# Performance work log

Hardware: AMD Instinct MI355X
Metric: run time of the kernel (lower is better)

Reference implementation:

```python
import jax, jax.numpy as jnp
import numpy as np

N = 50000
E = 800000
C = 128   # embed_channels
H = 4     # num_heads
D = C // H
POS = 3


def setup_inputs() -> dict:
    key = jax.random.key(0)
    ks = jax.random.split(key, 8)
    feat = jax.random.normal(ks[0], (N, C), dtype=jnp.float32)
    coord = jax.random.normal(ks[1], (N, POS), dtype=jnp.float32)
    graph = jax.random.randint(ks[2], (2, E), 0, N, dtype=jnp.int32)
    qkv_w = jax.random.normal(ks[3], (3 * C, C), dtype=jnp.float32) * (1.0 / np.sqrt(C))
    qkv_b = jax.random.normal(ks[4], (3 * C,), dtype=jnp.float32) * 0.02
    rpe_w = jax.random.normal(ks[5], (C, POS), dtype=jnp.float32) * (1.0 / np.sqrt(POS))
    rpe_b = jax.random.normal(ks[6], (C,), dtype=jnp.float32) * 0.02
    return {"feat": feat, "coord": coord, "graph": graph,
            "qkv_w": qkv_w, "qkv_b": qkv_b, "rpe_w": rpe_w, "rpe_b": rpe_b}


def _segment_softmax(x, seg, n):
    # x: [E, H], seg: [E] -> softmax over edges sharing the same destination node
    seg_max = jax.ops.segment_max(x, seg, num_segments=n)          # [N, H]
    seg_max = jnp.where(jnp.isfinite(seg_max), seg_max, 0.0)
    ex = jnp.exp(x - seg_max[seg])                                 # [E, H]
    seg_sum = jax.ops.segment_sum(ex, seg, num_segments=n)         # [N, H]
    return ex / seg_sum[seg]


def reference(feat, coord, graph, qkv_w, qkv_b, rpe_w, rpe_b):
    n = feat.shape[0]
    # qkv projection: [N, 3C] -> [N, 3, H, D]
    qkv = (feat @ qkv_w.T + qkv_b).reshape(n, 3, H, D)
    query, key, value = qkv[:, 0], qkv[:, 1], qkv[:, 2]            # each [N, H, D]
    dst, src = graph[0], graph[1]                                  # [E]
    # relative position encoding per edge
    rel = coord[dst] - coord[src]                                  # [E, 3]
    rpe = (rel @ rpe_w.T + rpe_b).reshape(-1, H, D)                # [E, H, D]
    # per-edge attention logits
    attn = (key[src] * query[dst] + rpe).sum(-1)                   # [E, H]
    attn = _segment_softmax(attn, dst, n)                          # [E, H]
    # weighted scatter-sum of values
    msg = attn[..., None] * value[src]                             # [E, H, D]
    out = jax.ops.segment_sum(msg, dst, num_segments=n)            # [N, H, D]
    return out.reshape(n, H * D)
```

## Files before the change

### kernel.cpp

```cpp
#include <hip/hip_runtime.h>
#include <hip/hip_bf16.h>

#define NN 50000
#define NE 800000
#define PAD 64
#define CONVB 6298

typedef _Float16 fp16x8 __attribute__((ext_vector_type(8)));
typedef _Float16 half2 __attribute__((ext_vector_type(2)));
typedef __attribute__((ext_vector_type(8))) unsigned short ushort8;
typedef __attribute__((ext_vector_type(4))) float f32x4;

static __device__ __forceinline__ unsigned short f2h(float x) {
    _Float16 h = (_Float16)x;
    return __builtin_bit_cast(unsigned short, h);
}
static __device__ __forceinline__ float dot2(half2 a, half2 b, float c) {
#if __has_builtin(__builtin_amdgcn_fdot2)
    return __builtin_amdgcn_fdot2(a, b, c, false);
#else
    return c + (float)a.x * (float)b.x + (float)a.y * (float)b.y;
#endif
}

__global__ __launch_bounds__(256) void k_pre(
    const float* __restrict__ feat, const float* __restrict__ w,
    unsigned short* __restrict__ feat16, unsigned short* __restrict__ w16,
    const float* __restrict__ coord, const float* __restrict__ rpe_w,
    const float* __restrict__ rpe_b, float* __restrict__ ca,
    float* __restrict__ cb)
{
    const int b = blockIdx.x;
    if (b < CONVB) {
        const int totalA = NN * 128 / 4;
        int idx = b * 256 + threadIdx.x;
        if (idx < totalA) {
            float4 a = ((const float4*)feat)[idx];
            ((ushort4*)feat16)[idx] = make_ushort4(f2h(a.x), f2h(a.y), f2h(a.z), f2h(a.w));
        } else {
            int k = idx - totalA;
            float4 a = ((const float4*)w)[k];
            ((ushort4*)w16)[k] = make_ushort4(f2h(a.x), f2h(a.y), f2h(a.z), f2h(a.w));
        }
        return;
    }
    __shared__ float s_rw[12];
    __shared__ float s_rb[4];
    if (threadIdx.x < 12) {
        int h = threadIdx.x / 3, p = threadIdx.x % 3;
        float s = 0.f;
        for (int d = 0; d < 32; ++d) s += rpe_w[(h * 32 + d) * 3 + p];
        s_rw[threadIdx.x] = s;
    } else if (threadIdx.x < 16) {
        int h = threadIdx.x - 12;
        float s = 0.f;
        for (int d = 0; d < 32; ++d) s += rpe_b[h * 32 + d];
        s_rb[h] = s;
    }
    __syncthreads();
    int n = (b - CONVB) * 256 + threadIdx.x;
    if (n < NN) {
        float c0 = coord[n * 3 + 0], c1 = coord[n * 3 + 1], c2 = coord[n * 3 + 2];
#pragma unroll
        for (int h = 0; h < 4; ++h) {
            float a = c0 * s_rw[h * 3 + 0] + c1 * s_rw[h * 3 + 1] + c2 * s_rw[h * 3 + 2];
            ca[n * 4 + h] = a;
            cb[n * 4 + h] = a + s_rb[h];
        }
    }
}

__global__ __launch_bounds__(256) void qkv_gemm(
    const unsigned short* __restrict__ feat16, const unsigned short* __restrict__ w16,
    const float* __restrict__ bias, unsigned short* __restrict__ qbuf16,
    unsigned short* __restrict__ kvbuf,
    const int* __restrict__ graph, int* __restrict__ cnt,
    int* __restrict__ sorted_src)
{
    const int role = blockIdx.x & 3;
    const int bi   = blockIdx.x >> 2;
    if (role == 3) {
        int t = threadIdx.x;
        for (int e = bi * 256 + t; e < NE; e += 391 * 256) {
            int dst = graph[e];
            int src = graph[NE + e];
            int slot = atomicAdd(&cnt[dst], 1);
            if (slot < PAD) sorted_src[(dst << 6) + slot] = src << 9;
        }
        return;
    }

    __shared__ __align__(16) unsigned short Ah[128][40];
    __shared__ __align__(16) unsigned short Bh[128][40];

    const int t  = threadIdx.x;
    const int bm = bi * 128;
    const int bc = role * 128;

    const int wave = t >> 6;
    const int lane = t & 63;
    const int wr = wave & 1;
    const int wc = wave >> 1;
    const int qd = lane >> 4;
    const int l15 = lane & 15;

    f32x4 acc[4][4];
#pragma unroll
    for (int i = 0; i < 4; ++i)
#pragma unroll
        for (int j = 0; j < 4; ++j)
            acc[i][j] = (f32x4){0.f, 0.f, 0.f, 0.f};

    for (int ks = 0; ks < 4; ++ks) {
        const int k0 = ks * 32;
        if (ks) __syncthreads();
#pragma unroll
        for (int c = 0; c < 2; ++c) {
            int idx = c * 256 + t;
            int r  = idx >> 2;
            int c8 = (idx & 3) * 8;
            int ga = bm + r;
            ushort8 a8 = (ga < NN)
                ? *(const ushort8*)(feat16 + (size_t)ga * 128 + k0 + c8)
                : (ushort8){0,0,0,0,0,0,0,0};
            *(ushort8*)&Ah[r][c8] = a8;
            *(ushort8*)&Bh[r][c8] = *(const ushort8*)(w16 + (size_t)(bc + r) * 128 + k0 + c8);
        }
        __syncthreads();
        fp16x8 af[4];
#pragma unroll
        for (int i = 0; i < 4; ++i)
            af[i] = *(const fp16x8*)&Ah[wr * 64 + 16 * i + l15][qd * 8];
#pragma unroll
        for (int j = 0; j < 4; ++j) {
            fp16x8 bf = *(const fp16x8*)&Bh[wc * 64 + 16 * j + l15][qd * 8];
#pragma unroll
            for (int i = 0; i < 4; ++i)
                acc[i][j] = __builtin_amdgcn_mfma_f32_16x16x32_f16(af[i], bf, acc[i][j], 0, 0, 0);
        }
    }

    float bj[4];
#pragma unroll
    for (int j = 0; j < 4; ++j)
        bj[j] = bias[bc + wc * 64 + 16 * j + l15];

    const int isQ = (role == 0);
    const int half = (role == 1) ? 0 : 128;
#pragma unroll
    for (int i = 0; i < 4; ++i) {
#pragma unroll
        for (int rg = 0; rg < 4; ++rg) {
            int row = bm + wr * 64 + 16 * i + qd * 4 + rg;
            if (row >= NN) continue;
#pragma unroll
            for (int j = 0; j < 4; ++j) {
                float v = acc[i][j][rg] + bj[j];
                int col = wc * 64 + 16 * j + l15;
                if (isQ) qbuf16[(size_t)row * 128 + col] = f2h(v);
                else     kvbuf[(size_t)row * 256 + half + col] = f2h(v);
            }
        }
    }
}

__global__ __launch_bounds__(256) void node_attn(
    const unsigned short* __restrict__ qbuf16, const unsigned short* __restrict__ kvbuf,
    const float* __restrict__ ca, const float* __restrict__ cb,
    const int* __restrict__ cnt, const int* __restrict__ sorted_src,
    float* __restrict__ out)
{
    const int t = threadIdx.x;
    const int n = blockIdx.x * 8 + (t >> 5);
    if (n >= NN) return;
    const int j = t & 31;
    const int h = j >> 3;
    const int j8 = j * 8;
    const int h4 = h * 4;

    const uint2 qv = *(const uint2*)((const char*)qbuf16 + (size_t)n * 256 + j8);
    const half2 qh01 = __builtin_bit_cast(half2, qv.x);
    const half2 qh23 = __builtin_bit_cast(half2, qv.y);
    const float cbh = cb[n * 4 + h];
    const int start = n << 6;
    int d = cnt[n];
    if (d > PAD) d = PAD;

    float4 acc = make_float4(0.f, 0.f, 0.f, 0.f);
    float den = 0.f;
    const char* kvp = (const char*)kvbuf;
    const char* cap = (const char*)ca;

    int i = 0;
    for (; i + 3 < d; i += 4) {
        int o0 = sorted_src[start + i];
        int o1 = sorted_src[start + i + 1];
        int o2 = sorted_src[start + i + 2];
        int o3 = sorted_src[start + i + 3];
        uint2 k0 = *(const uint2*)(kvp + (unsigned)o0 + j8);
        uint2 k1 = *(const uint2*)(kvp + (unsigned)o1 + j8);
        uint2 k2 = *(const uint2*)(kvp + (unsigned)o2 + j8);
        uint2 k3 = *(const uint2*)(kvp + (unsigned)o3 + j8);
        uint2 v0 = *(const uint2*)(kvp + (unsigned)o0 + 256 + j8);
        uint2 v1 = *(const uint2*)(kvp + (unsigned)o1 + 256 + j8);
        uint2 v2 = *(const uint2*)(kvp + (unsigned)o2 + 256 + j8);
        uint2 v3 = *(const uint2*)(kvp + (unsigned)o3 + 256 + j8);
        float a0 = *(const float*)(cap + ((unsigned)o0 >> 5) + h4);
        float a1 = *(const float*)(cap + ((unsigned)o1 >> 5) + h4);
        float a2 = *(const float*)(cap + ((unsigned)o2 >> 5) + h4);
        float a3 = *(const float*)(cap + ((unsigned)o3 >> 5) + h4);

        float p0 = dot2(qh01, __builtin_bit_cast(half2, k0.x),
                   dot2(qh23, __builtin_bit_cast(half2, k0.y), 0.f));
        float p1 = dot2(qh01, __builtin_bit_cast(half2, k1.x),
                   dot2(qh23, __builtin_bit_cast(half2, k1.y), 0.f));
        float p2 = dot2(qh01, __builtin_bit_cast(half2, k2.x),
                   dot2(qh23, __builtin_bit_cast(half2, k2.y), 0.f));
        float p3 = dot2(qh01, __builtin_bit_cast(half2, k3.x),
                   dot2(qh23, __builtin_bit_cast(half2, k3.y), 0.f));
        p0 += __shfl_xor(p0, 1); p1 += __shfl_xor(p1, 1);
        p2 += __shfl_xor(p2, 1); p3 += __shfl_xor(p3, 1);
        p0 += __shfl_xor(p0, 2); p1 += __shfl_xor(p1, 2);
        p2 += __shfl_xor(p2, 2); p3 += __shfl_xor(p3, 2);
        p0 += __shfl_xor(p0, 4); p1 += __shfl_xor(p1, 4);
        p2 += __shfl_xor(p2, 4); p3 += __shfl_xor(p3, 4);

        float e0 = __expf(p0 + cbh - a0);
        float e1 = __expf(p1 + cbh - a1);
        float e2 = __expf(p2 + cbh - a2);
        float e3 = __expf(p3 + cbh - a3);
        den += (e0 + e1) + (e2 + e3);
        half2 v0a = __builtin_bit_cast(half2, v0.x), v0b = __builtin_bit_cast(half2, v0.y);
        half2 v1a = __builtin_bit_cast(half2, v1.x), v1b = __builtin_bit_cast(half2, v1.y);
        half2 v2a = __builtin_bit_cast(half2, v2.x), v2b = __builtin_bit_cast(half2, v2.y);
        half2 v3a = __builtin_bit_cast(half2, v3.x), v3b = __builtin_bit_cast(half2, v3.y);
        acc.x += e0 * (float)v0a.x + e1 * (float)v1a.x + e2 * (float)v2a.x + e3 * (float)v3a.x;
        acc.y += e0 * (float)v0a.y + e1 * (float)v1a.y + e2 * (float)v2a.y + e3 * (float)v3a.y;
        acc.z += e0 * (float)v0b.x + e1 * (float)v1b.x + e2 * (float)v2b.x + e3 * (float)v3b.x;
        acc.w += e0 * (float)v0b.y + e1 * (float)v1b.y + e2 * (float)v2b.y + e3 * (float)v3b.y;
    }
    for (; i < d; ++i) {
        int o0 = sorted_src[start + i];
        uint2 k0 = *(const uint2*)(kvp + (unsigned)o0 + j8);
        uint2 v0 = *(const uint2*)(kvp + (unsigned)o0 + 256 + j8);
        float a0 = *(const float*)(cap + ((unsigned)o0 >> 5) + h4);
        float p0 = dot2(qh01, __builtin_bit_cast(half2, k0.x),
                   dot2(qh23, __builtin_bit_cast(half2, k0.y), 0.f));
        p0 += __shfl_xor(p0, 1);
        p0 += __shfl_xor(p0, 2);
        p0 += __shfl_xor(p0, 4);
        float e = __expf(p0 + cbh - a0);
        den += e;
        half2 va = __builtin_bit_cast(half2, v0.x);
        half2 vb = __builtin_bit_cast(half2, v0.y);
        acc.x += e * (float)va.x;
        acc.y += e * (float)va.y;
        acc.z += e * (float)vb.x;
        acc.w += e * (float)vb.y;
    }

    float inv = (den > 0.f) ? 1.0f / den : 0.f;
    float4 o = make_float4(acc.x * inv, acc.y * inv, acc.z * inv, acc.w * inv);
    ((float4*)(out + (size_t)n * 128))[j] = o;
}

extern "C" void kernel_launch(void* const* d_in, const int* in_sizes, int n_in,
                              void* d_out, int out_size, void* d_ws, size_t ws_size,
                              hipStream_t stream) {
    const float* feat  = (const float*)d_in[0];
    const float* coord = (const float*)d_in[1];
    const int*   graph = (const int*)d_in[2];
    const float* qkv_w = (const float*)d_in[3];
    const float* qkv_b = (const float*)d_in[4];
    const float* rpe_w = (const float*)d_in[5];
    const float* rpe_b = (const float*)d_in[6];
    float* out = (float*)d_out;

    unsigned short* qbuf16 = (unsigned short*)d_ws;
    unsigned short* kvbuf  = qbuf16 + (size_t)NN * 128;
    unsigned short* feat16 = kvbuf + (size_t)NN * 256;
    unsigned short* w16    = feat16 + (size_t)NN * 128;
    int*   cnt        = (int*)(w16 + 384 * 128);
    int*   sorted_src = cnt + NN;
    float* ca         = (float*)(sorted_src + (size_t)NN * PAD);
    float* cb         = ca + (size_t)NN * 4;

    hipMemsetAsync(cnt, 0, NN * sizeof(int), stream);

    k_pre    <<<dim3(CONVB + 196), 256, 0, stream>>>(feat, qkv_w, feat16, w16,
                                                     coord, rpe_w, rpe_b, ca, cb);
    qkv_gemm <<<dim3(391 * 4), 256, 0, stream>>>(feat16, w16, qkv_b, qbuf16, kvbuf,
                                                 graph, cnt, sorted_src);
    node_attn<<<dim3((NN + 7) / 8), 256, 0, stream>>>(qbuf16, kvbuf, ca, cb,
                                                      cnt, sorted_src, out);
}
```

Baseline: 214.2 us.

## Move edge bucketing into pre-kernel and stage GEMM output through LDS for vector stores

The edge-scatter work that builds per-destination source lists moves out of the GEMM kernel into the preprocessing kernel, where it runs first alongside the coordinate and fp16-conversion work. This leaves the GEMM grid with only its three compute roles. The GEMM epilogue now writes each 32-row slice of the accumulator tile into shared memory, then reads it back and stores it as 16-byte vectors, replacing scattered 2-byte stores. The cost is extra barriers and LDS round-trips per slice. The pre-kernel may also lengthen because atomic-heavy scatter blocks now sit on its critical path.

```diff
diff --git a/kernel.cpp b/kernel.cpp
--- a/kernel.cpp
+++ b/kernel.cpp
@@ -4,6 +4,8 @@
 #define NN 50000
 #define NE 800000
 #define PAD 64
+#define SCB 391
+#define CAB 196
 #define CONVB 6298
 
 typedef _Float16 fp16x8 __attribute__((ext_vector_type(8)));
@@ -28,60 +30,14 @@
     unsigned short* __restrict__ feat16, unsigned short* __restrict__ w16,
     const float* __restrict__ coord, const float* __restrict__ rpe_w,
     const float* __restrict__ rpe_b, float* __restrict__ ca,
-    float* __restrict__ cb)
-{
-    const int b = blockIdx.x;
-    if (b < CONVB) {
-        const int totalA = NN * 128 / 4;
-        int idx = b * 256 + threadIdx.x;
-        if (idx < totalA) {
-            float4 a = ((const float4*)feat)[idx];
-            ((ushort4*)feat16)[idx] = make_ushort4(f2h(a.x), f2h(a.y), f2h(a.z), f2h(a.w));
-        } else {
-            int k = idx - totalA;
-            float4 a = ((const float4*)w)[k];
-            ((ushort4*)w16)[k] = make_ushort4(f2h(a.x), f2h(a.y), f2h(a.z), f2h(a.w));
-        }
-        return;
-    }
-    __shared__ float s_rw[12];
-    __shared__ float s_rb[4];
-    if (threadIdx.x < 12) {
-        int h = threadIdx.x / 3, p = threadIdx.x % 3;
-        float s = 0.f;
-        for (int d = 0; d < 32; ++d) s += rpe_w[(h * 32 + d) * 3 + p];
-        s_rw[threadIdx.x] = s;
-    } else if (threadIdx.x < 16) {
-        int h = threadIdx.x - 12;
-        float s = 0.f;
-        for (int d = 0; d < 32; ++d) s += rpe_b[h * 32 + d];
-        s_rb[h] = s;
-    }
-    __syncthreads();
-    int n = (b - CONVB) * 256 + threadIdx.x;
-    if (n < NN) {
-        float c0 = coord[n * 3 + 0], c1 = coord[n * 3 + 1], c2 = coord[n * 3 + 2];
-#pragma unroll
-        for (int h = 0; h < 4; ++h) {
-            float a = c0 * s_rw[h * 3 + 0] + c1 * s_rw[h * 3 + 1] + c2 * s_rw[h * 3 + 2];
-            ca[n * 4 + h] = a;
-            cb[n * 4 + h] = a + s_rb[h];
-        }
-    }
-}
-
-__global__ __launch_bounds__(256) void qkv_gemm(
-    const unsigned short* __restrict__ feat16, const unsigned short* __restrict__ w16,
-    const float* __restrict__ bias, unsigned short* __restrict__ qbuf16,
-    unsigned short* __restrict__ kvbuf,
+    float* __restrict__ cb,
     const int* __restrict__ graph, int* __restrict__ cnt,
     int* __restrict__ sorted_src)
 {
-    const int role = blockIdx.x & 3;
-    const int bi   = blockIdx.x >> 2;
-    if (role == 3) {
-        int t = threadIdx.x;
-        for (int e = bi * 256 + t; e < NE; e += 391 * 256) {
+    const int b = blockIdx.x;
+    const int t = threadIdx.x;
+    if (b < SCB) {
+        for (int e = b * 256 + t; e < NE; e += SCB * 256) {
             int dst = graph[e];
             int src = graph[NE + e];
             int slot = atomicAdd(&cnt[dst], 1);
@@ -89,11 +45,56 @@
         }
         return;
     }
-
+    if (b < SCB + CAB) {
+        __shared__ float s_rw[12];
+        __shared__ float s_rb[4];
+        if (t < 12) {
+            int h = t / 3, p = t % 3;
+            float s = 0.f;
+            for (int d = 0; d < 32; ++d) s += rpe_w[(h * 32 + d) * 3 + p];
+            s_rw[t] = s;
+        } else if (t < 16) {
+            int h = t - 12;
+            float s = 0.f;
+            for (int d = 0; d < 32; ++d) s += rpe_b[h * 32 + d];
+            s_rb[h] = s;
+        }
+        __syncthreads();
+        int n = (b - SCB) * 256 + t;
+        if (n < NN) {
+            float c0 = coord[n * 3 + 0], c1 = coord[n * 3 + 1], c2 = coord[n * 3 + 2];
+#pragma unroll
+            for (int h = 0; h < 4; ++h) {
+                float a = c0 * s_rw[h * 3 + 0] + c1 * s_rw[h * 3 + 1] + c2 * s_rw[h * 3 + 2];
+                ca[n * 4 + h] = a;
+                cb[n * 4 + h] = a + s_rb[h];
+            }
+        }
+        return;
+    }
+    const int totalA = NN * 128 / 4;
+    int idx = (b - SCB - CAB) * 256 + t;
+    if (idx < totalA) {
+        float4 a = ((const float4*)feat)[idx];
+        ((ushort4*)feat16)[idx] = make_ushort4(f2h(a.x), f2h(a.y), f2h(a.z), f2h(a.w));
+    } else {
+        int k = idx - totalA;
+        float4 a = ((const float4*)w)[k];
+        ((ushort4*)w16)[k] = make_ushort4(f2h(a.x), f2h(a.y), f2h(a.z), f2h(a.w));
+    }
+}
+
+__global__ __launch_bounds__(256) void qkv_gemm(
+    const unsigned short* __restrict__ feat16, const unsigned short* __restrict__ w16,
+    const float* __restrict__ bias, unsigned short* __restrict__ qbuf16,
+    unsigned short* __restrict__ kvbuf)
+{
     __shared__ __align__(16) unsigned short Ah[128][40];
     __shared__ __align__(16) unsigned short Bh[128][40];
 
-    const int t  = threadIdx.x;
+    const int t    = threadIdx.x;
+    const int bi   = blockIdx.x / 3;
+    const int role = blockIdx.x - bi * 3;
     const int bm = bi * 128;
     const int bc = role * 128;
 
@@ -145,20 +146,31 @@
     for (int j = 0; j < 4; ++j)
         bj[j] = bias[bc + wc * 64 + 16 * j + l15];
 
+    unsigned short* Ct = &Ah[0][0];
     const int isQ = (role == 0);
     const int half = (role == 1) ? 0 : 128;
-#pragma unroll
+    const int relRowW = wr * 16 + qd * 4;
+
     for (int i = 0; i < 4; ++i) {
-#pragma unroll
-        for (int rg = 0; rg < 4; ++rg) {
-            int row = bm + wr * 64 + 16 * i + qd * 4 + rg;
-            if (row >= NN) continue;
-#pragma unroll
-            for (int j = 0; j < 4; ++j) {
-                float v = acc[i][j][rg] + bj[j];
-                int col = wc * 64 + 16 * j + l15;
-                if (isQ) qbuf16[(size_t)row * 128 + col] = f2h(v);
-                else     kvbuf[(size_t)row * 256 + half + col] = f2h(v);
+        __syncthreads();
+#pragma unroll
+        for (int j = 0; j < 4; ++j) {
+            int col = wc * 64 + 16 * j + l15;
+#pragma unroll
+            for (int rg = 0; rg < 4; ++rg)
+                Ct[(relRowW + rg) * 136 + col] = f2h(acc[i][j][rg] + bj[j]);
+        }
+        __syncthreads();
+#pragma unroll
+        for (int p = 0; p < 2; ++p) {
+            int linear = p * 256 + t;
+            int rr = linear >> 4;
+            int cc = linear & 15;
+            int absRow = bm + 16 * i + rr + ((rr >> 4) * 48);
+            if (absRow < NN) {
+                ushort8 val = *(const ushort8*)&Ct[rr * 136 + cc * 8];
+                if (isQ) *(ushort8*)(qbuf16 + (size_t)absRow * 128 + cc * 8) = val;
+                else     *(ushort8*)(kvbuf + (size_t)absRow * 256 + half + cc * 8) = val;
             }
         }
     }
@@ -287,10 +299,10 @@
 
     hipMemsetAsync(cnt, 0, NN * sizeof(int), stream);
 
-    k_pre    <<<dim3(CONVB + 196), 256, 0, stream>>>(feat, qkv_w, feat16, w16,
-                                                     coord, rpe_w, rpe_b, ca, cb);
-    qkv_gemm <<<dim3(391 * 4), 256, 0, stream>>>(feat16, w16, qkv_b, qbuf16, kvbuf,
-                                                 graph, cnt, sorted_src);
+    k_pre    <<<dim3(SCB + CAB + CONVB), 256, 0, stream>>>(feat, qkv_w, feat16, w16,
+                                                           coord, rpe_w, rpe_b, ca, cb,
+                                                           graph, cnt, sorted_src);
+    qkv_gemm <<<dim3(391 * 3), 256, 0, stream>>>(feat16, w16, qkv_b, qbuf16, kvbuf);
     node_attn<<<dim3((NN + 7) / 8), 256, 0, stream>>>(qbuf16, kvbuf, ca, cb,
                                                       cnt, sorted_src, out);
 }
```

Result: no change. 213.6 us (-0.3%).
